# Performance work log

Hardware: AMD Instinct MI355X
Metric: run time of the kernel (lower is better)

The kernel has to match this reference:

```python
import jax, jax.numpy as jnp
import numpy as np

D_MODEL = 2048
N_HEADS = 16
N_KV = 4
D_HEAD = D_MODEL // N_HEADS
N_GROUPS = N_HEADS // N_KV
THETA = 10000.0


def bitlinear(x, W):
    """BitNet b1.58 BitLinear: ternary weights (absmean scale) + 8-bit absmax activations (STE)."""
    sw = jnp.mean(jnp.abs(W)) + 1e-5
    Wq = jnp.clip(jnp.round(W / sw), -1.0, 1.0) * sw
    sx = 127.0 / jnp.clip(jnp.max(jnp.abs(x), axis=-1, keepdims=True), 1e-5, None)
    xq = jnp.clip(jnp.round(x * sx), -128.0, 127.0) / sx
    return jnp.einsum('bsd,od->bso', xq, Wq)


def rope_tables(seq, d_head, dtype=jnp.float32):
    freqs = 1.0 / (THETA ** (jnp.arange(0, d_head, 2, dtype=dtype) / d_head))
    t = jnp.arange(seq, dtype=dtype)
    ang = jnp.outer(t, freqs)  # [seq, d_head//2]
    return jnp.cos(ang), jnp.sin(ang)


def apply_rope(x, cos, sin):
    # x: [b, h, s, d]; cos/sin: [s, d//2] -> broadcast [1,1,s,d//2]
    c = cos[None, None]
    s = sin[None, None]
    x1, x2 = jnp.split(x, 2, axis=-1)
    return jnp.concatenate([x1 * c - x2 * s, x2 * c + x1 * s], axis=-1)


def setup_inputs() -> dict:
    key = jax.random.key(0)
    ks = jax.random.split(key, 5)
    return {
        'x': jax.random.normal(ks[0], (2, 2048, D_MODEL), jnp.float32),
        'Wq': jax.random.normal(ks[1], (D_MODEL, D_MODEL), jnp.float32) * 0.02,
        'Wk': jax.random.normal(ks[2], (N_KV * D_HEAD, D_MODEL), jnp.float32) * 0.02,
        'Wv': jax.random.normal(ks[3], (N_KV * D_HEAD, D_MODEL), jnp.float32) * 0.02,
        'Wo': jax.random.normal(ks[4], (D_MODEL, D_MODEL), jnp.float32) * 0.02,
    }


def reference(x, Wq, Wk, Wv, Wo):
    b, s, _ = x.shape
    q = bitlinear(x, Wq).reshape(b, s, N_HEADS, D_HEAD).transpose(0, 2, 1, 3)
    k = bitlinear(x, Wk).reshape(b, s, N_KV, D_HEAD).transpose(0, 2, 1, 3)
    v = bitlinear(x, Wv).reshape(b, s, N_KV, D_HEAD).transpose(0, 2, 1, 3)
    cos, sin = rope_tables(s, D_HEAD)
    q = apply_rope(q, cos, sin)
    k = apply_rope(k, cos, sin)
    # GQA without materializing expanded K/V: group query heads per kv head
    qg = q.reshape(b, N_KV, N_GROUPS, s, D_HEAD)
    scale = 1.0 / jnp.sqrt(jnp.asarray(D_HEAD, x.dtype))
    scores = jnp.einsum('bkgsd,bktd->bkgst', qg, k) * scale  # [b,kv,g,s,s]
    causal = jnp.triu(jnp.ones((s, s), dtype=bool), k=1)
    scores = jnp.where(causal[None, None, None], jnp.asarray(-jnp.inf, scores.dtype), scores)
    p = jax.nn.softmax(scores, axis=-1)
    out = jnp.einsum('bkgst,bktd->bkgsd', p, v)  # [b,kv,g,s,d]
    out = out.reshape(b, N_HEADS, s, D_HEAD).transpose(0, 2, 1, 3).reshape(b, s, D_MODEL)
    return bitlinear(out, Wo)
```

## Files before the change

kernel.cpp:

```cpp
#include <hip/hip_runtime.h>
#include <hip/hip_bf16.h>
#include <stdint.h>

typedef __bf16 bf16x8 __attribute__((ext_vector_type(8)));
typedef __bf16 bf16x4v __attribute__((ext_vector_type(4)));
typedef float f32x4 __attribute__((ext_vector_type(4)));
typedef unsigned short u16x8 __attribute__((ext_vector_type(8)));
typedef unsigned short u16x4 __attribute__((ext_vector_type(4)));

__device__ __forceinline__ unsigned short f2bf(float f) {
  union { float f; unsigned int u; } v; v.f = f;
  unsigned int r = v.u + 0x7fffu + ((v.u >> 16) & 1u);
  return (unsigned short)(r >> 16);
}

__device__ __forceinline__ f32x4 mfma16(bf16x8 a, bf16x8 b, f32x4 c) {
  return __builtin_amdgcn_mfma_f32_16x16x32_bf16(a, b, c, 0, 0, 0);
}

__device__ __forceinline__ void gload_lds16(const void* g, void* l) {
  __builtin_amdgcn_global_load_lds(
      (const __attribute__((address_space(1))) void*)g,
      (__attribute__((address_space(3))) void*)l, 16, 0, 0);
}

__global__ void absum_k(const float* __restrict__ w, long n4, float* __restrict__ out) {
  long i = (long)blockIdx.x * blockDim.x + threadIdx.x;
  long stride = (long)gridDim.x * blockDim.x;
  const float4* w4 = (const float4*)w;
  float s = 0.f;
  for (; i < n4; i += stride) {
    float4 v = w4[i];
    s += fabsf(v.x) + fabsf(v.y) + fabsf(v.z) + fabsf(v.w);
  }
  #pragma unroll
  for (int o = 32; o; o >>= 1) s += __shfl_down(s, o);
  __shared__ float sm[4];
  int lane = threadIdx.x & 63, wv = threadIdx.x >> 6;
  if (lane == 0) sm[wv] = s;
  __syncthreads();
  if (threadIdx.x == 0) atomicAdd(out, sm[0] + sm[1] + sm[2] + sm[3]);
}

__global__ void finalize_k(const float* __restrict__ sums, float* __restrict__ sw) {
  int i = threadIdx.x;
  if (i < 4) {
    const float inv[4] = {1.f/(2048.f*2048.f), 1.f/(512.f*2048.f),
                          1.f/(512.f*2048.f), 1.f/(2048.f*2048.f)};
    sw[i] = sums[i] * inv[i] + 1e-5f;
  }
}

__global__ void quantw_k(const float* __restrict__ w, unsigned short* __restrict__ o,
                         long n4, const float* __restrict__ swp) {
  float sw = *swp;
  long i = (long)blockIdx.x * blockDim.x + threadIdx.x;
  long stride = (long)gridDim.x * blockDim.x;
  const float4* w4 = (const float4*)w;
  u16x4* o4 = (u16x4*)o;
  for (; i < n4; i += stride) {
    float4 v = w4[i];
    u16x4 t;
    t[0] = f2bf(fminf(fmaxf(rintf(v.x / sw), -1.f), 1.f));
    t[1] = f2bf(fminf(fmaxf(rintf(v.y / sw), -1.f), 1.f));
    t[2] = f2bf(fminf(fmaxf(rintf(v.z / sw), -1.f), 1.f));
    t[3] = f2bf(fminf(fmaxf(rintf(v.w / sw), -1.f), 1.f));
    o4[i] = t;
  }
}

__global__ void ropetab_k(float* __restrict__ cosT, float* __restrict__ sinT) {
  int idx = blockIdx.x * 256 + threadIdx.x;
  int s = idx >> 6, d = idx & 63;
  float freq = expf(-(float)d * (9.210340371976184f / 64.0f));
  float ang = (float)s * freq;
  cosT[idx] = cosf(ang);
  sinT[idx] = sinf(ang);
}

__global__ __launch_bounds__(256) void quanta_k(const float* __restrict__ x,
                                                unsigned short* __restrict__ xq,
                                                float* __restrict__ rs) {
  int row = blockIdx.x;
  const float* xr = x + (size_t)row * 2048;
  int tid = threadIdx.x;
  float4 v0 = ((const float4*)xr)[tid * 2];
  float4 v1 = ((const float4*)xr)[tid * 2 + 1];
  float m = fmaxf(fmaxf(fmaxf(fabsf(v0.x), fabsf(v0.y)), fmaxf(fabsf(v0.z), fabsf(v0.w))),
                  fmaxf(fmaxf(fabsf(v1.x), fabsf(v1.y)), fmaxf(fabsf(v1.z), fabsf(v1.w))));
  #pragma unroll
  for (int o = 32; o; o >>= 1) m = fmaxf(m, __shfl_xor(m, o));
  __shared__ float sm[4];
  if ((tid & 63) == 0) sm[tid >> 6] = m;
  __syncthreads();
  m = fmaxf(fmaxf(sm[0], sm[1]), fmaxf(sm[2], sm[3]));
  float rm = fmaxf(m, 1e-5f);
  float sx = 127.0f / rm;
  float vv[8] = {v0.x, v0.y, v0.z, v0.w, v1.x, v1.y, v1.z, v1.w};
  u16x8 o8;
  #pragma unroll
  for (int j = 0; j < 8; j++) {
    float r = rintf(vv[j] * sx);
    r = fminf(fmaxf(r, -128.f), 127.f);
    o8[j] = f2bf(r);
  }
  ((u16x8*)(xq + (size_t)row * 2048))[tid] = o8;
  if (tid == 0) rs[row] = rm * (1.0f / 127.0f);
}

__global__ __launch_bounds__(256) void gemm_k(const unsigned short* __restrict__ A,
                                              const unsigned short* __restrict__ Bt,
                                              float* __restrict__ C,
                                              int M, int N, int K,
                                              const float* __restrict__ rowscale,
                                              const float* __restrict__ sw, int mode) {
  __shared__ unsigned short As[128 * 32];
  __shared__ unsigned short Bs[128 * 32];
  int tid = threadIdx.x;
  int lane = tid & 63, wv = tid >> 6;
  int g = lane >> 4, li = lane & 15;
  int wm = wv >> 1, wn = wv & 1;
  int L = blockIdx.x + gridDim.x * blockIdx.y;
  int nwg = gridDim.x * gridDim.y;
  int swz_id = (L & 7) * (nwg >> 3) + (L >> 3);
  int m0 = (swz_id / gridDim.x) * 128, n0 = (swz_id % gridDim.x) * 128;
  int sr = lane >> 2;
  int sc = lane & 3;
  int gc = (sc ^ ((sr >> 1) & 3)) * 8;
  int swz = (g ^ ((li >> 1) & 3)) * 8;
  f32x4 acc[4][4] = {};

  for (int k0 = 0; k0 < K; k0 += 32) {
    __syncthreads();
    #pragma unroll
    for (int j = 0; j < 2; j++) {
      int row = (wv * 2 + j) * 16 + sr;
      gload_lds16(&A[(size_t)(m0 + row) * K + k0 + gc], &As[(wv * 2 + j) * 512]);
      gload_lds16(&Bt[(size_t)(n0 + row) * K + k0 + gc], &Bs[(wv * 2 + j) * 512]);
    }
    __syncthreads();
    bf16x8 af[4], bfr[4];
    #pragma unroll
    for (int i = 0; i < 4; i++)
      af[i] = *(const bf16x8*)&As[(wm * 64 + i * 16 + li) * 32 + swz];
    #pragma unroll
    for (int j = 0; j < 4; j++)
      bfr[j] = *(const bf16x8*)&Bs[(wn * 64 + j * 16 + li) * 32 + swz];
    #pragma unroll
    for (int i = 0; i < 4; i++)
      #pragma unroll
      for (int j = 0; j < 4; j++)
        acc[i][j] = mfma16(af[i], bfr[j], acc[i][j]);
  }

  #pragma unroll
  for (int i = 0; i < 4; i++) {
    int row = m0 + wm * 64 + i * 16 + g * 4;
    #pragma unroll
    for (int j = 0; j < 4; j++) {
      int col = n0 + wn * 64 + j * 16 + li;
      float s = (mode == 0) ? ((col < 2048) ? sw[0] : (col < 2560 ? sw[1] : sw[2]))
                            : sw[3];
      #pragma unroll
      for (int r = 0; r < 4; r++)
        C[(size_t)(row + r) * N + col] = acc[i][j][r] * (rowscale[row + r] * s);
    }
  }
}

__global__ __launch_bounds__(256) void ropeapply_k(const float* __restrict__ raw,
                                                   const float* __restrict__ cosT,
                                                   const float* __restrict__ sinT,
                                                   unsigned short* __restrict__ qb,
                                                   unsigned short* __restrict__ kb) {
  const float CS = 0.1275356234f;
  int r = blockIdx.x;
  int b = r >> 11, s = r & 2047;
  const float* row = raw + (size_t)r * 3072;
  int tid = threadIdx.x;
  for (int idx = tid; idx < 1024; idx += 256) {
    int h = idx >> 6, d = idx & 63;
    float x1 = row[h * 128 + d], x2 = row[h * 128 + d + 64];
    float c = cosT[s * 64 + d], sn = sinT[s * 64 + d];
    size_t base = ((size_t)(b * 16 + h) * 2048 + s) * 128;
    qb[base + d]      = f2bf((x1 * c - x2 * sn) * CS);
    qb[base + d + 64] = f2bf((x2 * c + x1 * sn) * CS);
  }
  {
    int h = tid >> 6, d = tid & 63;
    float x1 = row[2048 + h * 128 + d], x2 = row[2048 + h * 128 + d + 64];
    float c = cosT[s * 64 + d], sn = sinT[s * 64 + d];
    size_t base = ((size_t)(b * 4 + h) * 2048 + s) * 128;
    kb[base + d]      = f2bf(x1 * c - x2 * sn);
    kb[base + d + 64] = f2bf(x2 * c + x1 * sn);
  }
}

__global__ __launch_bounds__(256) void transv_k(const float* __restrict__ raw,
                                                unsigned short* __restrict__ vtb) {
  __shared__ unsigned short T[128][136];
  int sc = blockIdx.x, hk = blockIdx.y, b = blockIdx.z;
  int tid = threadIdx.x;
  #pragma unroll
  for (int i = 0; i < 16; i++) {
    int idx4 = i * 256 + tid;
    int s = idx4 >> 5, d4 = idx4 & 31;
    float4 v = *(const float4*)&raw[((size_t)(b * 2048 + sc * 128 + s)) * 3072 +
                                    2560 + hk * 128 + d4 * 4];
    u16x4 t4;
    t4[0] = f2bf(v.x); t4[1] = f2bf(v.y); t4[2] = f2bf(v.z); t4[3] = f2bf(v.w);
    *(u16x4*)&T[s][d4 * 4] = t4;
  }
  __syncthreads();
  int d = tid >> 1, s0 = (tid & 1) * 64;
  size_t obase = ((size_t)(b * 4 + hk) * 128 + d) * 2048 + sc * 128 + s0;
  #pragma unroll
  for (int j = 0; j < 8; j++) {
    u16x8 o8;
    #pragma unroll
    for (int e = 0; e < 8; e++) o8[e] = T[s0 + j * 8 + e][d];
    *(u16x8*)&vtb[obase + j * 8] = o8;
  }
}

__global__ __launch_bounds__(256) void attn_k(const unsigned short* __restrict__ qb,
                                              const unsigned short* __restrict__ kb,
                                              const unsigned short* __restrict__ vtb,
                                              float* __restrict__ out) {
  int h = blockIdx.y, b = blockIdx.z;
  int wv = threadIdx.x >> 6, lane = threadIdx.x & 63;
  int g = lane >> 4, li = lane & 15;
  int kh = h >> 2;
  const unsigned short* qp = qb + ((size_t)(b * 16 + h) * 2048) * 128;
  const unsigned short* kp = kb + ((size_t)(b * 4 + kh) * 2048) * 128;
  const unsigned short* vp = vtb + ((size_t)(b * 4 + kh) * 128) * 2048;

  __shared__ unsigned short Ks[2][64 * 128];
  __shared__ unsigned short Vs[2][128 * 64];
  __shared__ unsigned short Pl[4][16][72];

  #pragma unroll 1
  for (int part = 0; part < 2; ++part) {
    int tq = part ? (31 - (int)blockIdx.x) : (int)blockIdx.x;
    int qw = tq * 64 + wv * 16;
    bf16x8 qf[4];
    #pragma unroll
    for (int kk = 0; kk < 4; kk++)
      qf[kk] = *(const bf16x8*)&qp[(size_t)(qw + li) * 128 + kk * 32 + g * 8];
    f32x4 oacc[8] = {};
    float mrun = -INFINITY, lrun = 0.f;
    int nt = tq + 1;

    {
      #pragma unroll
      for (int i = 0; i < 4; i++) {
        int r = wv * 16 + i * 4 + g;
        gload_lds16(kp + (size_t)r * 128 + ((li ^ (r & 7)) * 8),
                    &Ks[0][(wv * 16 + i * 4) * 128]);
      }
      #pragma unroll
      for (int i = 0; i < 4; i++) {
        int d = wv * 32 + i * 8 + (lane >> 3);
        gload_lds16(vp + (size_t)d * 2048 + (((lane & 7) ^ (d & 7)) * 8),
                    &Vs[0][(wv * 32 + i * 8) * 64]);
      }
    }

    #pragma unroll 1
    for (int t = 0; t < nt; ++t) {
      int cur = t & 1;
      if (t + 1 < nt) {
        int kv1 = (t + 1) * 64;
        #pragma unroll
        for (int i = 0; i < 4; i++) {
          int r = wv * 16 + i * 4 + g;
          gload_lds16(kp + (size_t)(kv1 + r) * 128 + ((li ^ (r & 7)) * 8),
                      &Ks[cur ^ 1][(wv * 16 + i * 4) * 128]);
        }
        #pragma unroll
        for (int i = 0; i < 4; i++) {
          int d = wv * 32 + i * 8 + (lane >> 3);
          gload_lds16(vp + (size_t)d * 2048 + kv1 + (((lane & 7) ^ (d & 7)) * 8),
                      &Vs[cur ^ 1][(wv * 32 + i * 8) * 64]);
        }
        asm volatile("s_waitcnt vmcnt(8)" ::: "memory");
      } else {
        asm volatile("s_waitcnt vmcnt(0)" ::: "memory");
      }
      __builtin_amdgcn_s_barrier();
      asm volatile("" ::: "memory");

      f32x4 st[4] = {};
      #pragma unroll
      for (int kk = 0; kk < 4; kk++) {
        #pragma unroll
        for (int n = 0; n < 4; n++) {
          bf16x8 kf = *(const bf16x8*)&Ks[cur][(n * 16 + li) * 128 +
                                              (((kk * 4 + g) ^ (li & 7)) * 8)];
          st[n] = mfma16(kf, qf[kk], st[n]);
        }
      }
      if (t == nt - 1) {
        int qrel = qw + li - t * 64;
        #pragma unroll
        for (int n = 0; n < 4; n++)
          #pragma unroll
          for (int r = 0; r < 4; r++)
            if ((n * 16 + g * 4 + r) > qrel) st[n][r] = -INFINITY;
      }
      float mx = st[0][0];
      #pragma unroll
      for (int n = 0; n < 4; n++)
        #pragma unroll
        for (int r = 0; r < 4; r++) mx = fmaxf(mx, st[n][r]);
      mx = fmaxf(mx, __shfl_xor(mx, 16));
      mx = fmaxf(mx, __shfl_xor(mx, 32));
      float mnew = fmaxf(mrun, mx);
      float alpha = exp2f(mrun - mnew);
      float lsum = 0.f;
      #pragma unroll
      for (int n = 0; n < 4; n++) {
        bf16x4v pw;
        #pragma unroll
        for (int r = 0; r < 4; r++) {
          float p = exp2f(st[n][r] - mnew);
          lsum += p;
          pw[r] = (__bf16)p;
        }
        *(bf16x4v*)&Pl[wv][li][n * 16 + g * 4] = pw;
      }
      lsum += __shfl_xor(lsum, 16);
      lsum += __shfl_xor(lsum, 32);
      lrun = lrun * alpha + lsum;
      mrun = mnew;
      if (__any(alpha != 1.0f)) {
        float ar[4];
        #pragma unroll
        for (int r = 0; r < 4; r++) ar[r] = __shfl(alpha, g * 4 + r, 64);
        #pragma unroll
        for (int dn = 0; dn < 8; dn++)
          #pragma unroll
          for (int r = 0; r < 4; r++) oacc[dn][r] *= ar[r];
      }
      __builtin_amdgcn_wave_barrier();
      bf16x8 pa0 = *(const bf16x8*)&Pl[wv][li][g * 8];
      bf16x8 pa1 = *(const bf16x8*)&Pl[wv][li][32 + g * 8];
      #pragma unroll
      for (int dn = 0; dn < 8; dn++) {
        int d = dn * 16 + li;
        bf16x8 vf0 = *(const bf16x8*)&Vs[cur][d * 64 + ((g ^ (li & 7)) * 8)];
        bf16x8 vf1 = *(const bf16x8*)&Vs[cur][d * 64 + (((4 + g) ^ (li & 7)) * 8)];
        oacc[dn] = mfma16(pa0, vf0, oacc[dn]);
        oacc[dn] = mfma16(pa1, vf1, oacc[dn]);
      }
      __builtin_amdgcn_wave_barrier();
      asm volatile("" ::: "memory");
      __builtin_amdgcn_s_barrier();
      asm volatile("" ::: "memory");
    }
    float linv = 1.0f / lrun;
    float lr_[4];
    #pragma unroll
    for (int r = 0; r < 4; r++) lr_[r] = __shfl(linv, g * 4 + r, 64);
    size_t obase = ((size_t)(b * 2048 + qw + g * 4)) * 2048 + h * 128;
    #pragma unroll
    for (int dn = 0; dn < 8; dn++)
      #pragma unroll
      for (int r = 0; r < 4; r++)
        out[obase + (size_t)r * 2048 + dn * 16 + li] = oacc[dn][r] * lr_[r];
  }
}

extern "C" void kernel_launch(void* const* d_in, const int* in_sizes, int n_in,
                              void* d_out, int out_size, void* d_ws, size_t ws_size,
                              hipStream_t stream) {
  const float* x  = (const float*)d_in[0];
  const float* Wq = (const float*)d_in[1];
  const float* Wk = (const float*)d_in[2];
  const float* Wv = (const float*)d_in[3];
  const float* Wo = (const float*)d_in[4];
  float* out = (float*)d_out;

  char* ws = (char*)d_ws;
  size_t off = 0;
  auto alloc = [&](size_t bytes) -> void* {
    void* p = ws + off;
    off = (off + bytes + 255) & ~(size_t)255;
    return p;
  };
  float* sums = (float*)alloc(16);
  float* sw   = (float*)alloc(16);
  float* rs   = (float*)alloc(4096 * 4);
  float* rs2  = (float*)alloc(4096 * 4);
  float* cosT = (float*)alloc((size_t)131072 * 4);
  float* sinT = (float*)alloc((size_t)131072 * 4);
  unsigned short* Wcat = (unsigned short*)alloc((size_t)3072 * 2048 * 2);
  unsigned short* Wot  = (unsigned short*)alloc((size_t)2048 * 2048 * 2);
  unsigned short* qb   = (unsigned short*)alloc((size_t)2 * 16 * 2048 * 128 * 2);
  unsigned short* kb   = (unsigned short*)alloc((size_t)2 * 4 * 2048 * 128 * 2);
  unsigned short* vtb  = (unsigned short*)alloc((size_t)2 * 4 * 128 * 2048 * 2);
  unsigned short* xq   = (unsigned short*)alloc((size_t)4096 * 2048 * 2);
  float* raw  = (float*)alloc((size_t)4096 * 3072 * 4);
  float* attn = raw;

  hipMemsetAsync(sums, 0, 16, stream);
  absum_k<<<256, 256, 0, stream>>>(Wq, (long)2048 * 2048 / 4, sums + 0);
  absum_k<<<128, 256, 0, stream>>>(Wk, (long)512 * 2048 / 4, sums + 1);
  absum_k<<<128, 256, 0, stream>>>(Wv, (long)512 * 2048 / 4, sums + 2);
  absum_k<<<256, 256, 0, stream>>>(Wo, (long)2048 * 2048 / 4, sums + 3);
  finalize_k<<<1, 4, 0, stream>>>(sums, sw);
  quantw_k<<<512, 256, 0, stream>>>(Wq, Wcat, (long)2048 * 2048 / 4, sw + 0);
  quantw_k<<<128, 256, 0, stream>>>(Wk, Wcat + (size_t)2048 * 2048, (long)512 * 2048 / 4, sw + 1);
  quantw_k<<<128, 256, 0, stream>>>(Wv, Wcat + (size_t)2560 * 2048, (long)512 * 2048 / 4, sw + 2);
  quantw_k<<<512, 256, 0, stream>>>(Wo, Wot, (long)2048 * 2048 / 4, sw + 3);
  ropetab_k<<<512, 256, 0, stream>>>(cosT, sinT);
  quanta_k<<<4096, 256, 0, stream>>>(x, xq, rs);
  dim3 g1(3072 / 128, 4096 / 128);
  gemm_k<<<g1, 256, 0, stream>>>(xq, Wcat, raw, 4096, 3072, 2048, rs, sw, 0);
  ropeapply_k<<<4096, 256, 0, stream>>>(raw, cosT, sinT, qb, kb);
  transv_k<<<dim3(16, 4, 2), 256, 0, stream>>>(raw, vtb);
  attn_k<<<dim3(16, 16, 2), 256, 0, stream>>>(qb, kb, vtb, attn);
  quanta_k<<<4096, 256, 0, stream>>>(attn, xq, rs2);
  dim3 g2(2048 / 128, 4096 / 128);
  gemm_k<<<g2, 256, 0, stream>>>(xq, Wot, out, 4096, 2048, 2048, rs2, sw, 1);
}
```

Before: 386.6 us.

## Switch bitlinear GEMMs to int8 MFMA and restructure attention tiling

Quantized activations and ternary weights are now stored as int8 and multiplied with the i32 16x16x64 int8 MFMA, which halves operand bytes and doubles K per instruction compared with bf16. The attention kernel drops the paired-tile scheme and launches one query tile per block on twice as many blocks, heaviest tiles first. It also single-buffers K, double-buffers V with a staggered prefetch, and keeps P in registers instead of round-tripping through LDS. The V transpose is permuted so the register P layout lines up with the MFMA operand order. The risks are load imbalance across blocks and exposed K load latency with only one K buffer.

```diff
diff --git a/kernel.cpp b/kernel.cpp
--- a/kernel.cpp
+++ b/kernel.cpp
@@ -3,10 +3,12 @@
 #include <stdint.h>
 
 typedef __bf16 bf16x8 __attribute__((ext_vector_type(8)));
-typedef __bf16 bf16x4v __attribute__((ext_vector_type(4)));
 typedef float f32x4 __attribute__((ext_vector_type(4)));
+typedef int i32x4 __attribute__((ext_vector_type(4)));
 typedef unsigned short u16x8 __attribute__((ext_vector_type(8)));
 typedef unsigned short u16x4 __attribute__((ext_vector_type(4)));
+typedef signed char i8x8 __attribute__((ext_vector_type(8)));
+typedef signed char i8x4 __attribute__((ext_vector_type(4)));
 
 __device__ __forceinline__ unsigned short f2bf(float f) {
   union { float f; unsigned int u; } v; v.f = f;
@@ -16,6 +18,10 @@
 
 __device__ __forceinline__ f32x4 mfma16(bf16x8 a, bf16x8 b, f32x4 c) {
   return __builtin_amdgcn_mfma_f32_16x16x32_bf16(a, b, c, 0, 0, 0);
+}
+
+__device__ __forceinline__ i32x4 mfma_i8(i32x4 a, i32x4 b, i32x4 c) {
+  return __builtin_amdgcn_mfma_i32_16x16x64_i8(a, b, c, 0, 0, 0);
 }
 
 __device__ __forceinline__ void gload_lds16(const void* g, void* l) {
@@ -51,20 +57,20 @@
   }
 }
 
-__global__ void quantw_k(const float* __restrict__ w, unsigned short* __restrict__ o,
+__global__ void quantw_k(const float* __restrict__ w, signed char* __restrict__ o,
                          long n4, const float* __restrict__ swp) {
   float sw = *swp;
   long i = (long)blockIdx.x * blockDim.x + threadIdx.x;
   long stride = (long)gridDim.x * blockDim.x;
   const float4* w4 = (const float4*)w;
-  u16x4* o4 = (u16x4*)o;
+  i8x4* o4 = (i8x4*)o;
   for (; i < n4; i += stride) {
     float4 v = w4[i];
-    u16x4 t;
-    t[0] = f2bf(fminf(fmaxf(rintf(v.x / sw), -1.f), 1.f));
-    t[1] = f2bf(fminf(fmaxf(rintf(v.y / sw), -1.f), 1.f));
-    t[2] = f2bf(fminf(fmaxf(rintf(v.z / sw), -1.f), 1.f));
-    t[3] = f2bf(fminf(fmaxf(rintf(v.w / sw), -1.f), 1.f));
+    i8x4 t;
+    t[0] = (signed char)(int)fminf(fmaxf(rintf(v.x / sw), -1.f), 1.f);
+    t[1] = (signed char)(int)fminf(fmaxf(rintf(v.y / sw), -1.f), 1.f);
+    t[2] = (signed char)(int)fminf(fmaxf(rintf(v.z / sw), -1.f), 1.f);
+    t[3] = (signed char)(int)fminf(fmaxf(rintf(v.w / sw), -1.f), 1.f);
     o4[i] = t;
   }
 }
@@ -79,7 +85,7 @@
 }
 
 __global__ __launch_bounds__(256) void quanta_k(const float* __restrict__ x,
-                                                unsigned short* __restrict__ xq,
+                                                signed char* __restrict__ xq,
                                                 float* __restrict__ rs) {
   int row = blockIdx.x;
   const float* xr = x + (size_t)row * 2048;
@@ -97,25 +103,25 @@
   float rm = fmaxf(m, 1e-5f);
   float sx = 127.0f / rm;
   float vv[8] = {v0.x, v0.y, v0.z, v0.w, v1.x, v1.y, v1.z, v1.w};
-  u16x8 o8;
+  i8x8 o8;
   #pragma unroll
   for (int j = 0; j < 8; j++) {
     float r = rintf(vv[j] * sx);
     r = fminf(fmaxf(r, -128.f), 127.f);
-    o8[j] = f2bf(r);
-  }
-  ((u16x8*)(xq + (size_t)row * 2048))[tid] = o8;
+    o8[j] = (signed char)(int)r;
+  }
+  ((i8x8*)(xq + (size_t)row * 2048))[tid] = o8;
   if (tid == 0) rs[row] = rm * (1.0f / 127.0f);
 }
 
-__global__ __launch_bounds__(256) void gemm_k(const unsigned short* __restrict__ A,
-                                              const unsigned short* __restrict__ Bt,
+__global__ __launch_bounds__(256) void gemm_k(const signed char* __restrict__ A,
+                                              const signed char* __restrict__ Bt,
                                               float* __restrict__ C,
                                               int M, int N, int K,
                                               const float* __restrict__ rowscale,
                                               const float* __restrict__ sw, int mode) {
-  __shared__ unsigned short As[128 * 32];
-  __shared__ unsigned short Bs[128 * 32];
+  __shared__ alignas(16) signed char As[128 * 64];
+  __shared__ alignas(16) signed char Bs[128 * 64];
   int tid = threadIdx.x;
   int lane = tid & 63, wv = tid >> 6;
   int g = lane >> 4, li = lane & 15;
@@ -126,31 +132,31 @@
   int m0 = (swz_id / gridDim.x) * 128, n0 = (swz_id % gridDim.x) * 128;
   int sr = lane >> 2;
   int sc = lane & 3;
-  int gc = (sc ^ ((sr >> 1) & 3)) * 8;
-  int swz = (g ^ ((li >> 1) & 3)) * 8;
-  f32x4 acc[4][4] = {};
-
-  for (int k0 = 0; k0 < K; k0 += 32) {
+  int gc = (sc ^ ((sr >> 1) & 3)) * 16;
+  int swz = (g ^ ((li >> 1) & 3)) * 16;
+  i32x4 acc[4][4] = {};
+
+  for (int k0 = 0; k0 < K; k0 += 64) {
     __syncthreads();
     #pragma unroll
     for (int j = 0; j < 2; j++) {
       int row = (wv * 2 + j) * 16 + sr;
-      gload_lds16(&A[(size_t)(m0 + row) * K + k0 + gc], &As[(wv * 2 + j) * 512]);
-      gload_lds16(&Bt[(size_t)(n0 + row) * K + k0 + gc], &Bs[(wv * 2 + j) * 512]);
+      gload_lds16(&A[(size_t)(m0 + row) * K + k0 + gc], &As[(wv * 2 + j) * 1024]);
+      gload_lds16(&Bt[(size_t)(n0 + row) * K + k0 + gc], &Bs[(wv * 2 + j) * 1024]);
     }
     __syncthreads();
-    bf16x8 af[4], bfr[4];
+    i32x4 af[4], bfr[4];
     #pragma unroll
     for (int i = 0; i < 4; i++)
-      af[i] = *(const bf16x8*)&As[(wm * 64 + i * 16 + li) * 32 + swz];
+      af[i] = *(const i32x4*)&As[(wm * 64 + i * 16 + li) * 64 + swz];
     #pragma unroll
     for (int j = 0; j < 4; j++)
-      bfr[j] = *(const bf16x8*)&Bs[(wn * 64 + j * 16 + li) * 32 + swz];
+      bfr[j] = *(const i32x4*)&Bs[(wn * 64 + j * 16 + li) * 64 + swz];
     #pragma unroll
     for (int i = 0; i < 4; i++)
       #pragma unroll
       for (int j = 0; j < 4; j++)
-        acc[i][j] = mfma16(af[i], bfr[j], acc[i][j]);
+        acc[i][j] = mfma_i8(af[i], bfr[j], acc[i][j]);
   }
 
   #pragma unroll
@@ -163,7 +169,7 @@
                             : sw[3];
       #pragma unroll
       for (int r = 0; r < 4; r++)
-        C[(size_t)(row + r) * N + col] = acc[i][j][r] * (rowscale[row + r] * s);
+        C[(size_t)(row + r) * N + col] = (float)acc[i][j][r] * (rowscale[row + r] * s);
     }
   }
 }
@@ -218,7 +224,10 @@
   for (int j = 0; j < 8; j++) {
     u16x8 o8;
     #pragma unroll
-    for (int e = 0; e < 8; e++) o8[e] = T[s0 + j * 8 + e][d];
+    for (int e = 0; e < 8; e++) {
+      int kvp = (j >> 2) * 32 + (e >> 2) * 16 + (j & 3) * 4 + (e & 3);
+      o8[e] = T[s0 + kvp][d];
+    }
     *(u16x8*)&vtb[obase + j * 8] = o8;
   }
 }
@@ -227,6 +236,7 @@
                                               const unsigned short* __restrict__ kb,
                                               const unsigned short* __restrict__ vtb,
                                               float* __restrict__ out) {
+  int tq = 31 - (int)blockIdx.x;
   int h = blockIdx.y, b = blockIdx.z;
   int wv = threadIdx.x >> 6, lane = threadIdx.x & 63;
   int g = lane >> 4, li = lane & 15;
@@ -235,140 +245,133 @@
   const unsigned short* kp = kb + ((size_t)(b * 4 + kh) * 2048) * 128;
   const unsigned short* vp = vtb + ((size_t)(b * 4 + kh) * 128) * 2048;
 
-  __shared__ unsigned short Ks[2][64 * 128];
+  __shared__ unsigned short Ks[64 * 128];
   __shared__ unsigned short Vs[2][128 * 64];
-  __shared__ unsigned short Pl[4][16][72];
+
+  int qw = tq * 64 + wv * 16;
+  int nt = tq + 1;
+  bf16x8 qf[4];
+  #pragma unroll
+  for (int kk = 0; kk < 4; kk++)
+    qf[kk] = *(const bf16x8*)&qp[(size_t)(qw + li) * 128 + kk * 32 + g * 8];
+  f32x4 oacc[8] = {};
+  float mrun = -INFINITY, lrun = 0.f;
+
+  #define STAGE_K(T_) do {                                                  \
+    int kv0_ = (T_) * 64;                                                   \
+    _Pragma("unroll")                                                       \
+    for (int i_ = 0; i_ < 4; i_++) {                                        \
+      int r_ = wv * 16 + i_ * 4 + g;                                        \
+      gload_lds16(kp + (size_t)(kv0_ + r_) * 128 + ((li ^ (r_ & 7)) * 8),   \
+                  &Ks[(wv * 16 + i_ * 4) * 128]);                           \
+    } } while (0)
+  #define STAGE_V(T_, BUF_) do {                                            \
+    int kv0_ = (T_) * 64;                                                   \
+    _Pragma("unroll")                                                       \
+    for (int i_ = 0; i_ < 4; i_++) {                                        \
+      int d_ = wv * 32 + i_ * 8 + (lane >> 3);                              \
+      gload_lds16(vp + (size_t)d_ * 2048 + kv0_ + (((lane & 7) ^ (d_ & 7)) * 8), \
+                  &Vs[BUF_][(wv * 32 + i_ * 8) * 64]);                      \
+    } } while (0)
+
+  STAGE_K(0);
+  STAGE_V(0, 0);
+  if (nt > 1) STAGE_V(1, 1);
 
   #pragma unroll 1
-  for (int part = 0; part < 2; ++part) {
-    int tq = part ? (31 - (int)blockIdx.x) : (int)blockIdx.x;
-    int qw = tq * 64 + wv * 16;
-    bf16x8 qf[4];
-    #pragma unroll
-    for (int kk = 0; kk < 4; kk++)
-      qf[kk] = *(const bf16x8*)&qp[(size_t)(qw + li) * 128 + kk * 32 + g * 8];
-    f32x4 oacc[8] = {};
-    float mrun = -INFINITY, lrun = 0.f;
-    int nt = tq + 1;
-
-    {
-      #pragma unroll
-      for (int i = 0; i < 4; i++) {
-        int r = wv * 16 + i * 4 + g;
-        gload_lds16(kp + (size_t)r * 128 + ((li ^ (r & 7)) * 8),
-                    &Ks[0][(wv * 16 + i * 4) * 128]);
+  for (int t = 0; t < nt; ++t) {
+    if (t == nt - 1) asm volatile("s_waitcnt vmcnt(0)" ::: "memory");
+    else             asm volatile("s_waitcnt vmcnt(4)" ::: "memory");
+    __builtin_amdgcn_s_barrier();
+    asm volatile("" ::: "memory");
+
+    f32x4 st[4] = {};
+    #pragma unroll
+    for (int kk = 0; kk < 4; kk++) {
+      #pragma unroll
+      for (int n = 0; n < 4; n++) {
+        bf16x8 kf = *(const bf16x8*)&Ks[(n * 16 + li) * 128 +
+                                        (((kk * 4 + g) ^ (li & 7)) * 8)];
+        st[n] = mfma16(kf, qf[kk], st[n]);
       }
-      #pragma unroll
-      for (int i = 0; i < 4; i++) {
-        int d = wv * 32 + i * 8 + (lane >> 3);
-        gload_lds16(vp + (size_t)d * 2048 + (((lane & 7) ^ (d & 7)) * 8),
-                    &Vs[0][(wv * 32 + i * 8) * 64]);
-      }
-    }
-
-    #pragma unroll 1
-    for (int t = 0; t < nt; ++t) {
-      int cur = t & 1;
-      if (t + 1 < nt) {
-        int kv1 = (t + 1) * 64;
-        #pragma unroll
-        for (int i = 0; i < 4; i++) {
-          int r = wv * 16 + i * 4 + g;
-          gload_lds16(kp + (size_t)(kv1 + r) * 128 + ((li ^ (r & 7)) * 8),
-                      &Ks[cur ^ 1][(wv * 16 + i * 4) * 128]);
-        }
-        #pragma unroll
-        for (int i = 0; i < 4; i++) {
-          int d = wv * 32 + i * 8 + (lane >> 3);
-          gload_lds16(vp + (size_t)d * 2048 + kv1 + (((lane & 7) ^ (d & 7)) * 8),
-                      &Vs[cur ^ 1][(wv * 32 + i * 8) * 64]);
-        }
-        asm volatile("s_waitcnt vmcnt(8)" ::: "memory");
-      } else {
-        asm volatile("s_waitcnt vmcnt(0)" ::: "memory");
-      }
-      __builtin_amdgcn_s_barrier();
-      asm volatile("" ::: "memory");
-
-      f32x4 st[4] = {};
-      #pragma unroll
-      for (int kk = 0; kk < 4; kk++) {
-        #pragma unroll
-        for (int n = 0; n < 4; n++) {
-          bf16x8 kf = *(const bf16x8*)&Ks[cur][(n * 16 + li) * 128 +
-                                              (((kk * 4 + g) ^ (li & 7)) * 8)];
-          st[n] = mfma16(kf, qf[kk], st[n]);
-        }
-      }
-      if (t == nt - 1) {
-        int qrel = qw + li - t * 64;
-        #pragma unroll
-        for (int n = 0; n < 4; n++)
-          #pragma unroll
-          for (int r = 0; r < 4; r++)
-            if ((n * 16 + g * 4 + r) > qrel) st[n][r] = -INFINITY;
-      }
-      float mx = st[0][0];
+    }
+
+    asm volatile("" ::: "memory");
+    __builtin_amdgcn_s_barrier();
+    asm volatile("" ::: "memory");
+    if (t + 1 < nt) STAGE_K(t + 1);
+
+    if (t == nt - 1) {
+      int qrel = qw + li - t * 64;
       #pragma unroll
       for (int n = 0; n < 4; n++)
         #pragma unroll
-        for (int r = 0; r < 4; r++) mx = fmaxf(mx, st[n][r]);
-      mx = fmaxf(mx, __shfl_xor(mx, 16));
-      mx = fmaxf(mx, __shfl_xor(mx, 32));
-      float mnew = fmaxf(mrun, mx);
-      float alpha = exp2f(mrun - mnew);
-      float lsum = 0.f;
-      #pragma unroll
-      for (int n = 0; n < 4; n++) {
-        bf16x4v pw;
+        for (int r = 0; r < 4; r++)
+          if ((n * 16 + g * 4 + r) > qrel) st[n][r] = -INFINITY;
+    }
+    float mx = st[0][0];
+    #pragma unroll
+    for (int n = 0; n < 4; n++)
+      #pragma unroll
+      for (int r = 0; r < 4; r++) mx = fmaxf(mx, st[n][r]);
+    mx = fmaxf(mx, __shfl_xor(mx, 16));
+    mx = fmaxf(mx, __shfl_xor(mx, 32));
+    float mnew = fmaxf(mrun, mx);
+    float alpha = exp2f(mrun - mnew);
+    float lsum = 0.f;
+    bf16x8 pa0, pa1;
+    #pragma unroll
+    for (int n = 0; n < 4; n++) {
+      #pragma unroll
+      for (int r = 0; r < 4; r++) {
+        float p = exp2f(st[n][r] - mnew);
+        lsum += p;
+        if (n < 2) pa0[(n & 1) * 4 + r] = (__bf16)p;
+        else       pa1[(n & 1) * 4 + r] = (__bf16)p;
+      }
+    }
+    lsum += __shfl_xor(lsum, 16);
+    lsum += __shfl_xor(lsum, 32);
+    lrun = lrun * alpha + lsum;
+    mrun = mnew;
+    if (__any(alpha != 1.0f)) {
+      float ar[4];
+      #pragma unroll
+      for (int r = 0; r < 4; r++) ar[r] = __shfl(alpha, g * 4 + r, 64);
+      #pragma unroll
+      for (int dn = 0; dn < 8; dn++)
         #pragma unroll
-        for (int r = 0; r < 4; r++) {
-          float p = exp2f(st[n][r] - mnew);
-          lsum += p;
-          pw[r] = (__bf16)p;
-        }
-        *(bf16x4v*)&Pl[wv][li][n * 16 + g * 4] = pw;
-      }
-      lsum += __shfl_xor(lsum, 16);
-      lsum += __shfl_xor(lsum, 32);
-      lrun = lrun * alpha + lsum;
-      mrun = mnew;
-      if (__any(alpha != 1.0f)) {
-        float ar[4];
-        #pragma unroll
-        for (int r = 0; r < 4; r++) ar[r] = __shfl(alpha, g * 4 + r, 64);
-        #pragma unroll
-        for (int dn = 0; dn < 8; dn++)
-          #pragma unroll
-          for (int r = 0; r < 4; r++) oacc[dn][r] *= ar[r];
-      }
-      __builtin_amdgcn_wave_barrier();
-      bf16x8 pa0 = *(const bf16x8*)&Pl[wv][li][g * 8];
-      bf16x8 pa1 = *(const bf16x8*)&Pl[wv][li][32 + g * 8];
-      #pragma unroll
-      for (int dn = 0; dn < 8; dn++) {
-        int d = dn * 16 + li;
-        bf16x8 vf0 = *(const bf16x8*)&Vs[cur][d * 64 + ((g ^ (li & 7)) * 8)];
-        bf16x8 vf1 = *(const bf16x8*)&Vs[cur][d * 64 + (((4 + g) ^ (li & 7)) * 8)];
-        oacc[dn] = mfma16(pa0, vf0, oacc[dn]);
-        oacc[dn] = mfma16(pa1, vf1, oacc[dn]);
-      }
-      __builtin_amdgcn_wave_barrier();
-      asm volatile("" ::: "memory");
-      __builtin_amdgcn_s_barrier();
-      asm volatile("" ::: "memory");
-    }
-    float linv = 1.0f / lrun;
-    float lr_[4];
-    #pragma unroll
-    for (int r = 0; r < 4; r++) lr_[r] = __shfl(linv, g * 4 + r, 64);
-    size_t obase = ((size_t)(b * 2048 + qw + g * 4)) * 2048 + h * 128;
-    #pragma unroll
-    for (int dn = 0; dn < 8; dn++)
-      #pragma unroll
-      for (int r = 0; r < 4; r++)
-        out[obase + (size_t)r * 2048 + dn * 16 + li] = oacc[dn][r] * lr_[r];
-  }
+        for (int r = 0; r < 4; r++) oacc[dn][r] *= ar[r];
+    }
+
+    int cur = t & 1;
+    #pragma unroll
+    for (int dn = 0; dn < 8; dn++) {
+      int d = dn * 16 + li;
+      bf16x8 vf0 = *(const bf16x8*)&Vs[cur][d * 64 + ((g ^ (li & 7)) * 8)];
+      bf16x8 vf1 = *(const bf16x8*)&Vs[cur][d * 64 + (((4 + g) ^ (li & 7)) * 8)];
+      oacc[dn] = mfma16(pa0, vf0, oacc[dn]);
+      oacc[dn] = mfma16(pa1, vf1, oacc[dn]);
+    }
+
+    asm volatile("" ::: "memory");
+    __builtin_amdgcn_s_barrier();
+    asm volatile("" ::: "memory");
+    if (t + 2 < nt) STAGE_V(t + 2, cur);
+  }
+  #undef STAGE_K
+  #undef STAGE_V
+
+  float linv = 1.0f / lrun;
+  float lr_[4];
+  #pragma unroll
+  for (int r = 0; r < 4; r++) lr_[r] = __shfl(linv, g * 4 + r, 64);
+  size_t obase = ((size_t)(b * 2048 + qw + g * 4)) * 2048 + h * 128;
+  #pragma unroll
+  for (int dn = 0; dn < 8; dn++)
+    #pragma unroll
+    for (int r = 0; r < 4; r++)
+      out[obase + (size_t)r * 2048 + dn * 16 + li] = oacc[dn][r] * lr_[r];
 }
 
 extern "C" void kernel_launch(void* const* d_in, const int* in_sizes, int n_in,
@@ -394,12 +397,12 @@
   float* rs2  = (float*)alloc(4096 * 4);
   float* cosT = (float*)alloc((size_t)131072 * 4);
   float* sinT = (float*)alloc((size_t)131072 * 4);
-  unsigned short* Wcat = (unsigned short*)alloc((size_t)3072 * 2048 * 2);
-  unsigned short* Wot  = (unsigned short*)alloc((size_t)2048 * 2048 * 2);
+  signed char* Wcat = (signed char*)alloc((size_t)3072 * 2048);
+  signed char* Wot  = (signed char*)alloc((size_t)2048 * 2048);
   unsigned short* qb   = (unsigned short*)alloc((size_t)2 * 16 * 2048 * 128 * 2);
   unsigned short* kb   = (unsigned short*)alloc((size_t)2 * 4 * 2048 * 128 * 2);
   unsigned short* vtb  = (unsigned short*)alloc((size_t)2 * 4 * 128 * 2048 * 2);
-  unsigned short* xq   = (unsigned short*)alloc((size_t)4096 * 2048 * 2);
+  signed char* xq   = (signed char*)alloc((size_t)4096 * 2048);
   float* raw  = (float*)alloc((size_t)4096 * 3072 * 4);
   float* attn = raw;
 
@@ -419,7 +422,7 @@
   gemm_k<<<g1, 256, 0, stream>>>(xq, Wcat, raw, 4096, 3072, 2048, rs, sw, 0);
   ropeapply_k<<<4096, 256, 0, stream>>>(raw, cosT, sinT, qb, kb);
   transv_k<<<dim3(16, 4, 2), 256, 0, stream>>>(raw, vtb);
-  attn_k<<<dim3(16, 16, 2), 256, 0, stream>>>(qb, kb, vtb, attn);
+  attn_k<<<dim3(32, 16, 2), 256, 0, stream>>>(qb, kb, vtb, attn);
   quanta_k<<<4096, 256, 0, stream>>>(attn, xq, rs2);
   dim3 g2(2048 / 128, 4096 / 128);
   gemm_k<<<g2, 256, 0, stream>>>(xq, Wot, out, 4096, 2048, 2048, rs2, sw, 1);
```

Measured after the change: 378.2 us. 1.02x faster.
